# Optimization experiments

Hardware: AMD Instinct MI355X
Metric: run time of the kernel (lower is better)

Reference implementation:

```python
import jax, jax.numpy as jnp
import numpy as np

N_OUT = 4096
N_IN = 4096
N_SPARSE = int(0.1 * N_OUT)  # 409
B, S = 4, 4096


def setup_inputs() -> dict:
    key = jax.random.key(0)
    k1, k2 = jax.random.split(key)
    x = jax.random.normal(k1, (B, S, N_IN), dtype=jnp.float32)
    y = jnp.zeros((B, S, N_OUT), dtype=jnp.float32)
    sparse_values = jax.random.normal(k2, (N_SPARSE, N_IN), dtype=jnp.float32) * 0.02
    # fixed boolean mask over output columns, represented as unique sorted indices
    rng = np.random.default_rng(0)
    sparse_idx = jnp.asarray(np.sort(rng.permutation(N_OUT)[:N_SPARSE]), dtype=jnp.int32)
    return {"x": x, "y": y, "sparse_values": sparse_values, "sparse_idx": sparse_idx}


def reference(x, y, sparse_values, sparse_idx):
    # y[..., mask] = x @ sparse_values.T  (scatter GEMM result into fixed columns)
    proj = jnp.einsum('bsi,oi->bso', x, sparse_values)  # [B, S, n_sparse]
    return y.at[..., sparse_idx].set(proj)
```

## Files before the change

kernel.cpp:

```cpp
#include <hip/hip_runtime.h>
#include <hip/hip_bf16.h>
#include <stdint.h>

#define M_TOT 16384
#define K_TOT 4096
#define N_COLS 4096
#define NS 409
#define NP 448
#define BM 64
#define BK 64
#define NT (K_TOT / BK)

#define BS_BYTES (NP * BK * 2)
#define AS_BYTES (BM * BK * 4)
#define LDS_TOTAL (2 * BS_BYTES + 2 * AS_BYTES)

typedef __attribute__((ext_vector_type(4))) float f32x4;
typedef __attribute__((ext_vector_type(8))) short bf16x8;
typedef __attribute__((ext_vector_type(8))) unsigned short u16x8;

#define VMWAIT(N) asm volatile("s_waitcnt vmcnt(" #N ")" ::: "memory")
#define FULLWAIT() asm volatile("s_waitcnt vmcnt(0) lgkmcnt(0)" ::: "memory")
#define BAR() do { __builtin_amdgcn_s_barrier(); asm volatile("" ::: "memory"); } while (0)

__device__ inline unsigned short f2bf(float f) {
  unsigned u = __float_as_uint(f);
  u += 0x7FFFu + ((u >> 16) & 1u);
  return (unsigned short)(u >> 16);
}

__device__ inline bf16x8 pack_bf8(f32x4 lo, f32x4 hi) {
  bf16x8 r;
  r[0] = (short)f2bf(lo[0]); r[1] = (short)f2bf(lo[1]);
  r[2] = (short)f2bf(lo[2]); r[3] = (short)f2bf(lo[3]);
  r[4] = (short)f2bf(hi[0]); r[5] = (short)f2bf(hi[1]);
  r[6] = (short)f2bf(hi[2]); r[7] = (short)f2bf(hi[3]);
  return r;
}

__device__ inline void gload_lds16(const void* g, void* l) {
  __builtin_amdgcn_global_load_lds(
      (const __attribute__((address_space(1))) void*)g,
      (__attribute__((address_space(3))) void*)l, 16, 0, 0);
}

__global__ __launch_bounds__(256) void convert_w(const float* __restrict__ Wf,
                                                 unsigned short* __restrict__ Wb) {
  const int gt = blockIdx.x * 256 + threadIdx.x;
  const int row = gt >> 9;
  const int c8 = (gt & 511) << 3;
  u16x8 o;
  if (row < NS) {
    const f32x4 lo = *(const f32x4*)(Wf + (size_t)row * K_TOT + c8);
    const f32x4 hi = *(const f32x4*)(Wf + (size_t)row * K_TOT + c8 + 4);
    o = (u16x8)pack_bf8(lo, hi);
  } else {
#pragma unroll
    for (int i = 0; i < 8; ++i) o[i] = 0;
  }
  *(u16x8*)(Wb + (size_t)row * K_TOT + c8) = o;
}

template <bool PRECONV>
__global__ __launch_bounds__(512, 2) void gemm_fused(
    const float* __restrict__ X, const float* __restrict__ Wf,
    const unsigned short* __restrict__ Wb, const int* __restrict__ idx,
    float* __restrict__ OUT) {
  extern __shared__ char smem[];
  char* const B0 = smem;
  char* const B1 = smem + BS_BYTES;
  char* const A0 = smem + 2 * BS_BYTES;
  char* const A1 = smem + 2 * BS_BYTES + AS_BYTES;

  const int tid = threadIdx.x;
  const int lane = tid & 63;
  const int wv = tid >> 6;
  const int wm = wv >> 2;
  const int wn = wv & 3;
  const int l16 = lane & 15;
  const int kg = lane >> 4;
  const int row0 = blockIdx.x * BM;

  int cidx[7];
#pragma unroll
  for (int j = 0; j < 7; ++j) {
    const int n = wn * 112 + j * 16 + l16;
    cidx[j] = (n < NS) ? idx[n] : -1;
  }

  f32x4 acc[2][7] = {};

  auto stageA = [&](int t, char* Ab) {
#pragma unroll
    for (int c = 0; c < 2; ++c) {
      const int qa = wv * 2 + c;
      const int lin = qa * 1024 + lane * 16;
      const int row = lin >> 8;
      const int lw = (lin & 255) ^ ((row & 7) << 4);
      const float* src = X + (size_t)(row0 + row) * K_TOT + t * BK + (lw >> 2);
      gload_lds16(src, Ab + qa * 1024);
    }
  };
  auto stageB = [&](int t, char* Bb) {
    if (PRECONV) {
#pragma unroll
      for (int c = 0; c < 7; ++c) {
        const int q = wv * 7 + c;
        const int lin = q * 1024 + lane * 16;
        const int row = lin >> 7;
        const int lw = (lin & 127) ^ ((row & 7) << 4);
        const unsigned short* src = Wb + (size_t)row * K_TOT + t * BK + (lw >> 1);
        gload_lds16(src, Bb + q * 1024);
      }
    } else {
#pragma unroll
      for (int c = 0; c < 7; ++c) {
        const int id = c * 512 + tid;
        const int row = id >> 3, sl = id & 7;
        f32x4 lo = {}, hi = {};
        if (row < NS) {
          const float* s = Wf + (size_t)row * K_TOT + t * BK + sl * 8;
          lo = *(const f32x4*)s;
          hi = *(const f32x4*)(s + 4);
        }
        const int byte = (row * 128 + sl * 16) ^ ((row & 7) << 4);
        *(bf16x8*)(Bb + byte) = pack_bf8(lo, hi);
      }
    }
  };

  auto compute = [&](const char* Ab, const char* Bb) {
#pragma unroll
    for (int ks = 0; ks < 2; ++ks) {
      bf16x8 af[2];
#pragma unroll
      for (int i = 0; i < 2; ++i) {
        const int m = wm * 32 + i * 16 + l16;
        const int base = m * 256 + ks * 128 + kg * 32;
        const int sw = (m & 7) << 4;
        const f32x4 lo = *(const f32x4*)(Ab + (base ^ sw));
        const f32x4 hi = *(const f32x4*)(Ab + ((base + 16) ^ sw));
        af[i] = pack_bf8(lo, hi);
      }
      bf16x8 bfr[7];
#pragma unroll
      for (int j = 0; j < 7; ++j) {
        const int n = wn * 112 + j * 16 + l16;
        const int byte = (n * 128 + ks * 64 + kg * 16) ^ ((n & 7) << 4);
        bfr[j] = *(const bf16x8*)(Bb + byte);
      }
#pragma unroll
      for (int i = 0; i < 2; ++i)
#pragma unroll
        for (int j = 0; j < 7; ++j)
          acc[i][j] = __builtin_amdgcn_mfma_f32_16x16x32_bf16(af[i], bfr[j],
                                                              acc[i][j], 0, 0, 0);
    }
  };

  stageB(0, B0);
  stageA(0, A0);
#pragma unroll 1
  for (int t = 0; t < NT; ++t) {
    const int cur = t & 1;
    char* const Bc = cur ? B1 : B0;
    char* const Ac = cur ? A1 : A0;
    if (t < NT - 1) {
      char* const Bn = cur ? B0 : B1;
      char* const An = cur ? A0 : A1;
      stageB(t + 1, Bn);
      stageA(t + 1, An);
      if (PRECONV) { VMWAIT(9); } else { FULLWAIT(); }
    } else {
      FULLWAIT();
    }
    BAR();
    compute(Ac, Bc);
    BAR();
  }

  float* rowbuf = (float*)smem;
#pragma unroll 1
  for (int rb = 0; rb < 8; ++rb) {
#pragma unroll
    for (int z = 0; z < 16; ++z) {
      f32x4 zv = {};
      *(f32x4*)(rowbuf + z * 2048 + tid * 4) = zv;
    }
    __syncthreads();
#pragma unroll
    for (int i = 0; i < 2; ++i) {
#pragma unroll
      for (int q = 0; q < 4; ++q) {
        const int r = wm * 32 + i * 16 + kg * 4 + q;
        if ((r >> 3) == rb) {
          float* dst = rowbuf + (r & 7) * N_COLS;
#pragma unroll
          for (int j = 0; j < 7; ++j)
            if (cidx[j] >= 0) dst[cidx[j]] = acc[i][j][q];
        }
      }
    }
    __syncthreads();
    float* ob = OUT + (size_t)(row0 + rb * 8) * N_COLS;
#pragma unroll
    for (int z = 0; z < 16; ++z) {
      const int off = z * 2048 + tid * 4;
      *(f32x4*)(ob + off) = *(const f32x4*)(rowbuf + off);
    }
    __syncthreads();
  }
}

extern "C" void kernel_launch(void* const* d_in, const int* in_sizes, int n_in,
                              void* d_out, int out_size, void* d_ws, size_t ws_size,
                              hipStream_t stream) {
  const float* x = (const float*)d_in[0];
  const float* w = (const float*)d_in[2];
  const int* idx = (const int*)d_in[3];
  float* out = (float*)d_out;

  const size_t need = (size_t)NP * K_TOT * 2;
  if (ws_size >= need) {
    unsigned short* wb = (unsigned short*)d_ws;
    convert_w<<<NP * K_TOT / 8 / 256, 256, 0, stream>>>(w, wb);
    hipFuncSetAttribute(reinterpret_cast<const void*>(&gemm_fused<true>),
                        hipFuncAttributeMaxDynamicSharedMemorySize, LDS_TOTAL);
    gemm_fused<true><<<M_TOT / BM, 512, LDS_TOTAL, stream>>>(x, w, wb, idx, out);
  } else {
    hipFuncSetAttribute(reinterpret_cast<const void*>(&gemm_fused<false>),
                        hipFuncAttributeMaxDynamicSharedMemorySize, LDS_TOTAL);
    gemm_fused<false><<<M_TOT / BM, 512, LDS_TOTAL, stream>>>(x, w, nullptr, idx, out);
  }
}
```

Measured before the change: 158.5 us.

## Convert A tile to bf16 once in registers and use 4 waves with larger per-wave tiles

```diff
diff --git a/kernel.cpp b/kernel.cpp
--- a/kernel.cpp
+++ b/kernel.cpp
@@ -12,7 +12,7 @@
 #define NT (K_TOT / BK)
 
 #define BS_BYTES (NP * BK * 2)
-#define AS_BYTES (BM * BK * 4)
+#define AS_BYTES (BM * BK * 2)
 #define LDS_TOTAL (2 * BS_BYTES + 2 * AS_BYTES)
 
 typedef __attribute__((ext_vector_type(4))) float f32x4;
@@ -21,6 +21,7 @@
 
 #define VMWAIT(N) asm volatile("s_waitcnt vmcnt(" #N ")" ::: "memory")
 #define FULLWAIT() asm volatile("s_waitcnt vmcnt(0) lgkmcnt(0)" ::: "memory")
+#define LGKM0() asm volatile("s_waitcnt lgkmcnt(0)" ::: "memory")
 #define BAR() do { __builtin_amdgcn_s_barrier(); asm volatile("" ::: "memory"); } while (0)
 
 __device__ inline unsigned short f2bf(float f) {
@@ -62,7 +63,7 @@
 }
 
 template <bool PRECONV>
-__global__ __launch_bounds__(512, 2) void gemm_fused(
+__global__ __launch_bounds__(256, 1) void gemm_fused(
     const float* __restrict__ X, const float* __restrict__ Wf,
     const unsigned short* __restrict__ Wb, const int* __restrict__ idx,
     float* __restrict__ OUT) {
@@ -75,37 +76,28 @@
   const int tid = threadIdx.x;
   const int lane = tid & 63;
   const int wv = tid >> 6;
-  const int wm = wv >> 2;
-  const int wn = wv & 3;
   const int l16 = lane & 15;
   const int kg = lane >> 4;
   const int row0 = blockIdx.x * BM;
 
+  const int arow = tid >> 2;
+  const int akseg = tid & 3;
+
   int cidx[7];
 #pragma unroll
   for (int j = 0; j < 7; ++j) {
-    const int n = wn * 112 + j * 16 + l16;
+    const int n = wv * 112 + j * 16 + l16;
     cidx[j] = (n < NS) ? idx[n] : -1;
   }
 
-  f32x4 acc[2][7] = {};
-
-  auto stageA = [&](int t, char* Ab) {
-#pragma unroll
-    for (int c = 0; c < 2; ++c) {
-      const int qa = wv * 2 + c;
-      const int lin = qa * 1024 + lane * 16;
-      const int row = lin >> 8;
-      const int lw = (lin & 255) ^ ((row & 7) << 4);
-      const float* src = X + (size_t)(row0 + row) * K_TOT + t * BK + (lw >> 2);
-      gload_lds16(src, Ab + qa * 1024);
-    }
-  };
+  f32x4 acc[4][7] = {};
+  f32x4 rg0[4], rg1[4];
+
   auto stageB = [&](int t, char* Bb) {
     if (PRECONV) {
 #pragma unroll
-      for (int c = 0; c < 7; ++c) {
-        const int q = wv * 7 + c;
+      for (int c = 0; c < 14; ++c) {
+        const int q = wv * 14 + c;
         const int lin = q * 1024 + lane * 16;
         const int row = lin >> 7;
         const int lw = (lin & 127) ^ ((row & 7) << 4);
@@ -114,8 +106,8 @@
       }
     } else {
 #pragma unroll
-      for (int c = 0; c < 7; ++c) {
-        const int id = c * 512 + tid;
+      for (int c = 0; c < 14; ++c) {
+        const int id = c * 256 + tid;
         const int row = id >> 3, sl = id & 7;
         f32x4 lo = {}, hi = {};
         if (row < NS) {
@@ -123,34 +115,41 @@
           lo = *(const f32x4*)s;
           hi = *(const f32x4*)(s + 4);
         }
-        const int byte = (row * 128 + sl * 16) ^ ((row & 7) << 4);
-        *(bf16x8*)(Bb + byte) = pack_bf8(lo, hi);
-      }
-    }
+        *(bf16x8*)(Bb + row * 128 + ((sl ^ (row & 7)) << 4)) = pack_bf8(lo, hi);
+      }
+    }
+  };
+
+  auto fillA = [&](int t, f32x4* r) {
+    const float* s = X + (size_t)(row0 + arow) * K_TOT + (t & 63) * BK + akseg * 16;
+    r[0] = *(const f32x4*)(s + 0);
+    r[1] = *(const f32x4*)(s + 4);
+    r[2] = *(const f32x4*)(s + 8);
+    r[3] = *(const f32x4*)(s + 12);
+  };
+  auto packA = [&](char* Ab, const f32x4* r) {
+    const int c0 = akseg * 2;
+    *(bf16x8*)(Ab + arow * 128 + (((c0) ^ (arow & 7)) << 4)) = pack_bf8(r[0], r[1]);
+    *(bf16x8*)(Ab + arow * 128 + (((c0 + 1) ^ (arow & 7)) << 4)) = pack_bf8(r[2], r[3]);
   };
 
   auto compute = [&](const char* Ab, const char* Bb) {
 #pragma unroll
     for (int ks = 0; ks < 2; ++ks) {
-      bf16x8 af[2];
-#pragma unroll
-      for (int i = 0; i < 2; ++i) {
-        const int m = wm * 32 + i * 16 + l16;
-        const int base = m * 256 + ks * 128 + kg * 32;
-        const int sw = (m & 7) << 4;
-        const f32x4 lo = *(const f32x4*)(Ab + (base ^ sw));
-        const f32x4 hi = *(const f32x4*)(Ab + ((base + 16) ^ sw));
-        af[i] = pack_bf8(lo, hi);
+      bf16x8 af[4];
+#pragma unroll
+      for (int i = 0; i < 4; ++i) {
+        const int m = i * 16 + l16;
+        af[i] = *(const bf16x8*)(Ab + m * 128 + ((((ks << 2) | kg) ^ (m & 7)) << 4));
       }
       bf16x8 bfr[7];
 #pragma unroll
       for (int j = 0; j < 7; ++j) {
-        const int n = wn * 112 + j * 16 + l16;
-        const int byte = (n * 128 + ks * 64 + kg * 16) ^ ((n & 7) << 4);
-        bfr[j] = *(const bf16x8*)(Bb + byte);
-      }
-#pragma unroll
-      for (int i = 0; i < 2; ++i)
+        const int n = wv * 112 + j * 16 + l16;
+        bfr[j] = *(const bf16x8*)(Bb + n * 128 + ((((ks << 2) | kg) ^ (n & 7)) << 4));
+      }
+#pragma unroll
+      for (int i = 0; i < 4; ++i)
 #pragma unroll
         for (int j = 0; j < 7; ++j)
           acc[i][j] = __builtin_amdgcn_mfma_f32_16x16x32_bf16(af[i], bfr[j],
@@ -159,53 +158,56 @@
   };
 
   stageB(0, B0);
-  stageA(0, A0);
+  fillA(0, rg0);
+  fillA(1, rg1);
+  VMWAIT(4);
+  packA(A0, rg0);
+
 #pragma unroll 1
-  for (int t = 0; t < NT; ++t) {
-    const int cur = t & 1;
-    char* const Bc = cur ? B1 : B0;
-    char* const Ac = cur ? A1 : A0;
-    if (t < NT - 1) {
-      char* const Bn = cur ? B0 : B1;
-      char* const An = cur ? A0 : A1;
-      stageB(t + 1, Bn);
-      stageA(t + 1, An);
-      if (PRECONV) { VMWAIT(9); } else { FULLWAIT(); }
-    } else {
-      FULLWAIT();
-    }
-    BAR();
-    compute(Ac, Bc);
-    BAR();
-  }
+  for (int t = 0; t < NT; t += 2) {
+    stageB((t + 1) & 63, B1);
+    fillA(t + 2, rg0);
+    VMWAIT(18);
+    packA(A1, rg1);
+    LGKM0();
+    BAR();
+    compute(A0, B0);
+    BAR();
+    stageB((t + 2) & 63, B0);
+    fillA(t + 3, rg1);
+    VMWAIT(18);
+    packA(A0, rg0);
+    LGKM0();
+    BAR();
+    compute(A1, B1);
+    BAR();
+  }
+  FULLWAIT();
+  BAR();
 
   float* rowbuf = (float*)smem;
-#pragma unroll 1
+#pragma unroll
   for (int rb = 0; rb < 8; ++rb) {
 #pragma unroll
-    for (int z = 0; z < 16; ++z) {
+    for (int z = 0; z < 32; ++z) {
       f32x4 zv = {};
-      *(f32x4*)(rowbuf + z * 2048 + tid * 4) = zv;
+      *(f32x4*)(rowbuf + z * 1024 + tid * 4) = zv;
     }
     __syncthreads();
-#pragma unroll
-    for (int i = 0; i < 2; ++i) {
+    if ((kg >> 1) == (rb & 1)) {
 #pragma unroll
       for (int q = 0; q < 4; ++q) {
-        const int r = wm * 32 + i * 16 + kg * 4 + q;
-        if ((r >> 3) == rb) {
-          float* dst = rowbuf + (r & 7) * N_COLS;
-#pragma unroll
-          for (int j = 0; j < 7; ++j)
-            if (cidx[j] >= 0) dst[cidx[j]] = acc[i][j][q];
-        }
+        float* dst = rowbuf + (((kg & 1) << 2) + q) * N_COLS;
+#pragma unroll
+        for (int j = 0; j < 7; ++j)
+          if (cidx[j] >= 0) dst[cidx[j]] = acc[rb >> 1][j][q];
       }
     }
     __syncthreads();
     float* ob = OUT + (size_t)(row0 + rb * 8) * N_COLS;
 #pragma unroll
-    for (int z = 0; z < 16; ++z) {
-      const int off = z * 2048 + tid * 4;
+    for (int z = 0; z < 32; ++z) {
+      const int off = z * 1024 + tid * 4;
       *(f32x4*)(ob + off) = *(const f32x4*)(rowbuf + off);
     }
     __syncthreads();
@@ -226,10 +228,10 @@
     convert_w<<<NP * K_TOT / 8 / 256, 256, 0, stream>>>(w, wb);
     hipFuncSetAttribute(reinterpret_cast<const void*>(&gemm_fused<true>),
                         hipFuncAttributeMaxDynamicSharedMemorySize, LDS_TOTAL);
-    gemm_fused<true><<<M_TOT / BM, 512, LDS_TOTAL, stream>>>(x, w, wb, idx, out);
+    gemm_fused<true><<<M_TOT / BM, 256, LDS_TOTAL, stream>>>(x, w, wb, idx, out);
   } else {
     hipFuncSetAttribute(reinterpret_cast<const void*>(&gemm_fused<false>),
                         hipFuncAttributeMaxDynamicSharedMemorySize, LDS_TOTAL);
-    gemm_fused<false><<<M_TOT / BM, 512, LDS_TOTAL, stream>>>(x, w, nullptr, idx, out);
-  }
-}
+    gemm_fused<false><<<M_TOT / BM, 256, LDS_TOTAL, stream>>>(x, w, nullptr, idx, out);
+  }
+}
```

Measured after the change: 175.2 us. 10.5% more time.

## Load A tile directly to registers with 1024-thread blocks, drop A LDS staging

Applied to the files above, without the earlier changes.

```diff
diff --git a/kernel.cpp b/kernel.cpp
--- a/kernel.cpp
+++ b/kernel.cpp
@@ -12,8 +12,7 @@
 #define NT (K_TOT / BK)
 
 #define BS_BYTES (NP * BK * 2)
-#define AS_BYTES (BM * BK * 4)
-#define LDS_TOTAL (2 * BS_BYTES + 2 * AS_BYTES)
+#define LDS_TOTAL (2 * BS_BYTES)
 
 typedef __attribute__((ext_vector_type(4))) float f32x4;
 typedef __attribute__((ext_vector_type(8))) short bf16x8;
@@ -62,24 +61,23 @@
 }
 
 template <bool PRECONV>
-__global__ __launch_bounds__(512, 2) void gemm_fused(
+__global__ __launch_bounds__(1024, 1) void gemm_fused(
     const float* __restrict__ X, const float* __restrict__ Wf,
     const unsigned short* __restrict__ Wb, const int* __restrict__ idx,
     float* __restrict__ OUT) {
   extern __shared__ char smem[];
   char* const B0 = smem;
   char* const B1 = smem + BS_BYTES;
-  char* const A0 = smem + 2 * BS_BYTES;
-  char* const A1 = smem + 2 * BS_BYTES + AS_BYTES;
 
   const int tid = threadIdx.x;
   const int lane = tid & 63;
   const int wv = tid >> 6;
-  const int wm = wv >> 2;
+  const int wq = wv >> 2;
   const int wn = wv & 3;
   const int l16 = lane & 15;
   const int kg = lane >> 4;
   const int row0 = blockIdx.x * BM;
+  const size_t arow = (size_t)(row0 + wq * 16 + l16);
 
   int cidx[7];
 #pragma unroll
@@ -88,124 +86,103 @@
     cidx[j] = (n < NS) ? idx[n] : -1;
   }
 
-  f32x4 acc[2][7] = {};
-
-  auto stageA = [&](int t, char* Ab) {
-#pragma unroll
-    for (int c = 0; c < 2; ++c) {
-      const int qa = wv * 2 + c;
-      const int lin = qa * 1024 + lane * 16;
-      const int row = lin >> 8;
-      const int lw = (lin & 255) ^ ((row & 7) << 4);
-      const float* src = X + (size_t)(row0 + row) * K_TOT + t * BK + (lw >> 2);
-      gload_lds16(src, Ab + qa * 1024);
-    }
-  };
+  f32x4 acc[7] = {};
+
   auto stageB = [&](int t, char* Bb) {
     if (PRECONV) {
-#pragma unroll
-      for (int c = 0; c < 7; ++c) {
-        const int q = wv * 7 + c;
-        const int lin = q * 1024 + lane * 16;
-        const int row = lin >> 7;
-        const int lw = (lin & 127) ^ ((row & 7) << 4);
-        const unsigned short* src = Wb + (size_t)row * K_TOT + t * BK + (lw >> 1);
-        gload_lds16(src, Bb + q * 1024);
+      if (wv < 14) {
+#pragma unroll
+        for (int c = 0; c < 4; ++c) {
+          const int q = wv * 4 + c;
+          const int rowp = lane >> 3;
+          const int p = lane & 7;
+          const int row = q * 8 + rowp;
+          const int s = p ^ rowp;
+          const unsigned short* src = Wb + (size_t)row * K_TOT + t * BK + s * 8;
+          gload_lds16(src, Bb + q * 1024);
+        }
       }
     } else {
 #pragma unroll
-      for (int c = 0; c < 7; ++c) {
-        const int id = c * 512 + tid;
-        const int row = id >> 3, sl = id & 7;
-        f32x4 lo = {}, hi = {};
-        if (row < NS) {
-          const float* s = Wf + (size_t)row * K_TOT + t * BK + sl * 8;
-          lo = *(const f32x4*)s;
-          hi = *(const f32x4*)(s + 4);
+      for (int c = 0; c < 4; ++c) {
+        const int id = c * 1024 + tid;
+        if (id < NP * 8) {
+          const int row = id >> 3, sl = id & 7;
+          f32x4 lo = {}, hi = {};
+          if (row < NS) {
+            const float* s = Wf + (size_t)row * K_TOT + t * BK + sl * 8;
+            lo = *(const f32x4*)s;
+            hi = *(const f32x4*)(s + 4);
+          }
+          *(bf16x8*)(Bb + row * 128 + ((sl ^ (row & 7)) << 4)) = pack_bf8(lo, hi);
         }
-        const int byte = (row * 128 + sl * 16) ^ ((row & 7) << 4);
-        *(bf16x8*)(Bb + byte) = pack_bf8(lo, hi);
       }
     }
   };
 
-  auto compute = [&](const char* Ab, const char* Bb) {
+  auto loadA = [&](int t, f32x4* rg) {
+    const float* s = X + arow * K_TOT + t * BK + kg * 8;
+    rg[0] = *(const f32x4*)(s + 0);
+    rg[1] = *(const f32x4*)(s + 4);
+    rg[2] = *(const f32x4*)(s + 32);
+    rg[3] = *(const f32x4*)(s + 36);
+  };
+
+  auto compute = [&](const char* Bb, const f32x4* rg) {
 #pragma unroll
     for (int ks = 0; ks < 2; ++ks) {
-      bf16x8 af[2];
-#pragma unroll
-      for (int i = 0; i < 2; ++i) {
-        const int m = wm * 32 + i * 16 + l16;
-        const int base = m * 256 + ks * 128 + kg * 32;
-        const int sw = (m & 7) << 4;
-        const f32x4 lo = *(const f32x4*)(Ab + (base ^ sw));
-        const f32x4 hi = *(const f32x4*)(Ab + ((base + 16) ^ sw));
-        af[i] = pack_bf8(lo, hi);
-      }
-      bf16x8 bfr[7];
+      const bf16x8 af = pack_bf8(rg[ks * 2], rg[ks * 2 + 1]);
 #pragma unroll
       for (int j = 0; j < 7; ++j) {
         const int n = wn * 112 + j * 16 + l16;
-        const int byte = (n * 128 + ks * 64 + kg * 16) ^ ((n & 7) << 4);
-        bfr[j] = *(const bf16x8*)(Bb + byte);
-      }
-#pragma unroll
-      for (int i = 0; i < 2; ++i)
-#pragma unroll
-        for (int j = 0; j < 7; ++j)
-          acc[i][j] = __builtin_amdgcn_mfma_f32_16x16x32_bf16(af[i], bfr[j],
-                                                              acc[i][j], 0, 0, 0);
+        const bf16x8 b = *(const bf16x8*)(
+            Bb + n * 128 + ((((ks << 2) | kg) ^ (n & 7)) << 4));
+        acc[j] = __builtin_amdgcn_mfma_f32_16x16x32_bf16(af, b, acc[j], 0, 0, 0);
+      }
     }
   };
 
   stageB(0, B0);
-  stageA(0, A0);
 #pragma unroll 1
   for (int t = 0; t < NT; ++t) {
-    const int cur = t & 1;
-    char* const Bc = cur ? B1 : B0;
-    char* const Ac = cur ? A1 : A0;
-    if (t < NT - 1) {
-      char* const Bn = cur ? B0 : B1;
-      char* const An = cur ? A0 : A1;
-      stageB(t + 1, Bn);
-      stageA(t + 1, An);
-      if (PRECONV) { VMWAIT(9); } else { FULLWAIT(); }
+    f32x4 rg[4];
+    loadA(t, rg);
+    stageB((t + 1) & (NT - 1), (t & 1) ? B0 : B1);
+    if (PRECONV) {
+      if (wv < 14) { VMWAIT(8); }
     } else {
       FULLWAIT();
     }
     BAR();
-    compute(Ac, Bc);
+    compute((t & 1) ? B1 : B0, rg);
     BAR();
   }
+  FULLWAIT();
+  BAR();
 
   float* rowbuf = (float*)smem;
 #pragma unroll 1
-  for (int rb = 0; rb < 8; ++rb) {
-#pragma unroll
-    for (int z = 0; z < 16; ++z) {
+  for (int rb = 0; rb < 16; ++rb) {
+#pragma unroll
+    for (int z = 0; z < 4; ++z) {
       f32x4 zv = {};
-      *(f32x4*)(rowbuf + z * 2048 + tid * 4) = zv;
+      *(f32x4*)(rowbuf + z * N_COLS + tid * 4) = zv;
     }
     __syncthreads();
-#pragma unroll
-    for (int i = 0; i < 2; ++i) {
+    if (4 * wq + kg == rb) {
 #pragma unroll
       for (int q = 0; q < 4; ++q) {
-        const int r = wm * 32 + i * 16 + kg * 4 + q;
-        if ((r >> 3) == rb) {
-          float* dst = rowbuf + (r & 7) * N_COLS;
-#pragma unroll
-          for (int j = 0; j < 7; ++j)
-            if (cidx[j] >= 0) dst[cidx[j]] = acc[i][j][q];
-        }
+        float* dst = rowbuf + q * N_COLS;
+#pragma unroll
+        for (int j = 0; j < 7; ++j)
+          if (cidx[j] >= 0) dst[cidx[j]] = acc[j][q];
       }
     }
     __syncthreads();
-    float* ob = OUT + (size_t)(row0 + rb * 8) * N_COLS;
-#pragma unroll
-    for (int z = 0; z < 16; ++z) {
-      const int off = z * 2048 + tid * 4;
+    float* ob = OUT + (size_t)(row0 + rb * 4) * N_COLS;
+#pragma unroll
+    for (int z = 0; z < 4; ++z) {
+      const int off = z * N_COLS + tid * 4;
       *(f32x4*)(ob + off) = *(const f32x4*)(rowbuf + off);
     }
     __syncthreads();
@@ -226,10 +203,10 @@
     convert_w<<<NP * K_TOT / 8 / 256, 256, 0, stream>>>(w, wb);
     hipFuncSetAttribute(reinterpret_cast<const void*>(&gemm_fused<true>),
                         hipFuncAttributeMaxDynamicSharedMemorySize, LDS_TOTAL);
-    gemm_fused<true><<<M_TOT / BM, 512, LDS_TOTAL, stream>>>(x, w, wb, idx, out);
+    gemm_fused<true><<<M_TOT / BM, 1024, LDS_TOTAL, stream>>>(x, w, wb, idx, out);
   } else {
     hipFuncSetAttribute(reinterpret_cast<const void*>(&gemm_fused<false>),
                         hipFuncAttributeMaxDynamicSharedMemorySize, LDS_TOTAL);
-    gemm_fused<false><<<M_TOT / BM, 512, LDS_TOTAL, stream>>>(x, w, nullptr, idx, out);
-  }
-}
+    gemm_fused<false><<<M_TOT / BM, 1024, LDS_TOTAL, stream>>>(x, w, nullptr, idx, out);
+  }
+}
```

After: 273.5 us. 72.6% more time.
